# Kernel tuning notes

Measured on AMD Instinct MI355X. Metric: run time of the kernel, lower is better.

The kernel has to match this reference:

```python
import jax, jax.numpy as jnp
import numpy as np

B, S, DIM, DA = 64, 4096, 256, 64
NEG = -1e30

def setup_inputs() -> dict:
    key = jax.random.key(0)
    k1, k2, k3, k4 = jax.random.split(key, 4)
    h = jax.random.normal(k1, (B, S, DIM), dtype=jnp.float32)
    mask = jax.random.randint(k2, (B, S), 0, 2).astype(jnp.bool_)
    # xavier_uniform with gain=1.414 as in the torch module
    lim_a = 1.414 * np.sqrt(6.0 / (DIM + DA))
    lim_b = 1.414 * np.sqrt(6.0 / (DA + 1))
    a = jax.random.uniform(k3, (DIM, DA), minval=-lim_a, maxval=lim_a, dtype=jnp.float32)
    b = jax.random.uniform(k4, (DA, 1), minval=-lim_b, maxval=lim_b, dtype=jnp.float32)
    return {"h": h, "mask": mask, "a": a, "b": b}

def reference(h, mask, a, b):
    # e: (B, S) additive-attention logits
    e = jnp.einsum('bsk,ko->bs', jnp.tanh(jnp.einsum('bsd,dk->bsk', h, a)), b)
    e = e + mask.astype(e.dtype) * NEG  # True == padding -> -1e30
    attn = jax.nn.softmax(e, axis=1)    # softmax over seq dim
    # weighted sum over seq: (B, DIM)
    return jnp.einsum('bs,bsd->bd', attn, h)
```

## Files before the change

kernel.cpp:

```cpp
#include <hip/hip_runtime.h>
#include <hip/hip_bf16.h>

#define B_      64
#define S_      4096
#define DIM_    256
#define DA_     64
#define NEG_    (-1e30f)
#define CHUNKS_ 16
#define ROWS_   256
#define NBLK_   256
#define TILES_TOT_ 16
#define LDW_    260
#define PSTR_   258

typedef _Float16 half8 __attribute__((ext_vector_type(8)));
typedef float float4v __attribute__((ext_vector_type(4)));

__device__ __forceinline__ float tanh_fast(float x) {
    float e = __expf(2.0f * x);
    return 1.0f - 2.0f * __builtin_amdgcn_rcpf(e + 1.0f);
}

__global__ __launch_bounds__(256) void prep_kernel(
    const float* __restrict__ a, const void* __restrict__ mask,
    _Float16* __restrict__ at_sw, int* __restrict__ flag)
{
    int idx = blockIdx.x * 256 + threadIdx.x;
    int j    = idx & 7;
    int lane = (idx >> 3) & 63;
    int kbnt = idx >> 9;
    int kb   = kbnt & 7;
    int nt   = kbnt >> 3;
    int d  = kb * 32 + (lane >> 4) * 8 + j;
    int kf = nt * 16 + (lane & 15);
    at_sw[idx] = (_Float16)a[d * DA_ + kf];

    if (blockIdx.x == 0) {
        __shared__ int anynz;
        if (threadIdx.x == 0) anynz = 0;
        __syncthreads();
        const unsigned char* mb = (const unsigned char*)mask;
        int base = threadIdx.x * 4;
        int v = mb[base + 1] | mb[base + 2] | mb[base + 3];
        if (v) atomicOr(&anynz, 1);
        __syncthreads();
        if (threadIdx.x == 0) *flag = (anynz == 0) ? 1 : 0;
    }
}

#define STAGE(ft_, sel_) do {                                                   \
    int cg_ = (int)blockIdx.x + ((ft_) >> 2) * NBLK_;                           \
    long long r0_ = (long long)(cg_ >> 4) * S_ + (long long)(cg_ & 15) * ROWS_  \
                  + ((ft_) & 3) * 64 + wave * 16;                               \
    const float* sp_ = h + r0_ * DIM_ + lane * 4;                               \
    _Pragma("unroll")                                                           \
    for (int i_ = 0; i_ < 16; ++i_) {                                           \
        __builtin_amdgcn_global_load_lds(                                       \
            (__attribute__((address_space(1))) void*)(sp_ + (size_t)i_ * DIM_), \
            (__attribute__((address_space(3))) void*)&buf[sel_][wave * 16 + i_][0], \
            16, 0, 0);                                                          \
    }                                                                           \
} while (0)

__global__ __launch_bounds__(256, 1) void fused_kernel(
    const float* __restrict__ h, const _Float16* __restrict__ at_sw,
    const float* __restrict__ bvec, const void* __restrict__ mask,
    const int* __restrict__ flag, float* __restrict__ part)
{
    __shared__ float buf[2][64][LDW_];

    const int t    = threadIdx.x;
    const int wave = t >> 6;
    const int lane = t & 63;
    const int quad = lane >> 4;
    const int nrow = lane & 15;
    const bool int32enc = (*flag != 0);

    half8 af[4][8];
    #pragma unroll
    for (int nt = 0; nt < 4; ++nt)
        #pragma unroll
        for (int kb = 0; kb < 8; ++kb)
            af[nt][kb] = *(const half8*)(at_sw + ((nt * 8 + kb) * 64 + lane) * 8);

    float4 bq[4];
    #pragma unroll
    for (int nt = 0; nt < 4; ++nt)
        bq[nt] = *(const float4*)(bvec + nt * 16 + quad * 4);

    float acc0 = 0.f, acc1 = 0.f, acc2 = 0.f, acc3 = 0.f;
    float m_w = NEG_, l_w = 0.f;

    STAGE(0, 0);
    asm volatile("s_waitcnt vmcnt(0)" ::: "memory");
    __builtin_amdgcn_sched_barrier(0);

    int cur = 0;
    #pragma unroll 1
    for (int ft = 0; ft < TILES_TOT_; ++ft) {
        int cg = (int)blockIdx.x + (ft >> 2) * NBLK_;
        long long row0 = (long long)(cg >> 4) * S_ + (long long)(cg & 15) * ROWS_
                       + (ft & 3) * 64 + wave * 16;

        long long mrow = row0 + nrow;
        int mv = int32enc ? ((const int*)mask)[mrow]
                          : (int)((const unsigned char*)mask)[mrow];

        if (ft < TILES_TOT_ - 1) STAGE(ft + 1, cur ^ 1);

        const float* hrow_l = &buf[cur][wave * 16 + nrow][0];
        float4v accm[4];
        #pragma unroll
        for (int nt = 0; nt < 4; ++nt) accm[nt] = (float4v){0.f, 0.f, 0.f, 0.f};
        #pragma unroll
        for (int kb = 0; kb < 8; ++kb) {
            float4 ha = *(const float4*)(hrow_l + kb * 32 + quad * 8);
            float4 hb2 = *(const float4*)(hrow_l + kb * 32 + quad * 8 + 4);
            union { _Float16 hh[8]; half8 v; } pk;
            pk.hh[0] = (_Float16)ha.x;  pk.hh[1] = (_Float16)ha.y;
            pk.hh[2] = (_Float16)ha.z;  pk.hh[3] = (_Float16)ha.w;
            pk.hh[4] = (_Float16)hb2.x; pk.hh[5] = (_Float16)hb2.y;
            pk.hh[6] = (_Float16)hb2.z; pk.hh[7] = (_Float16)hb2.w;
            #pragma unroll
            for (int nt = 0; nt < 4; ++nt)
                accm[nt] = __builtin_amdgcn_mfma_f32_16x16x32_f16(af[nt][kb], pk.v, accm[nt], 0, 0, 0);
        }

        float p = 0.f;
        #pragma unroll
        for (int nt = 0; nt < 4; ++nt) {
            p += tanh_fast(accm[nt][0]) * bq[nt].x;
            p += tanh_fast(accm[nt][1]) * bq[nt].y;
            p += tanh_fast(accm[nt][2]) * bq[nt].z;
            p += tanh_fast(accm[nt][3]) * bq[nt].w;
        }
        p += __shfl_xor(p, 16);
        p += __shfl_xor(p, 32);

        float ev = mv ? NEG_ : p;
        float mx = ev;
        mx = fmaxf(mx, __shfl_xor(mx, 1));
        mx = fmaxf(mx, __shfl_xor(mx, 2));
        mx = fmaxf(mx, __shfl_xor(mx, 4));
        mx = fmaxf(mx, __shfl_xor(mx, 8));
        float m_new = fmaxf(m_w, mx);
        float rs  = __expf(m_w - m_new);
        float w_s = __expf(ev - m_new);
        float sm = w_s;
        sm += __shfl_xor(sm, 1);
        sm += __shfl_xor(sm, 2);
        sm += __shfl_xor(sm, 4);
        sm += __shfl_xor(sm, 8);
        l_w = l_w * rs + sm;
        m_w = m_new;
        acc0 *= rs; acc1 *= rs; acc2 *= rs; acc3 *= rs;

        #pragma unroll
        for (int s = 0; s < 16; ++s) {
            float wv = __shfl(w_s, s);
            float4 hv = *(const float4*)(&buf[cur][wave * 16 + s][lane * 4]);
            acc0 = fmaf(wv, hv.x, acc0);
            acc1 = fmaf(wv, hv.y, acc1);
            acc2 = fmaf(wv, hv.z, acc2);
            acc3 = fmaf(wv, hv.w, acc3);
        }

        if ((ft & 3) == 3) {
            float* pc = part + (size_t)(cg * 4 + wave) * PSTR_;
            float4 o4 = make_float4(acc0, acc1, acc2, acc3);
            *(float4*)(pc + 2 + lane * 4) = o4;
            if (lane == 0) { pc[0] = m_w; pc[1] = l_w; }
            acc0 = acc1 = acc2 = acc3 = 0.f;
            m_w = NEG_; l_w = 0.f;
        }

        asm volatile("s_waitcnt vmcnt(0) lgkmcnt(0)" ::: "memory");
        __builtin_amdgcn_sched_barrier(0);
        cur ^= 1;
    }
}

__global__ __launch_bounds__(256) void merge_kernel(
    const float* __restrict__ part, float* __restrict__ out)
{
    const int b = blockIdx.x;
    const int t = threadIdx.x;
    const float* pb = part + (size_t)b * 64 * PSTR_;
    float M = NEG_;
    #pragma unroll
    for (int i = 0; i < 64; ++i) M = fmaxf(M, pb[i * PSTR_]);
    float L = 0.f, o = 0.f;
    #pragma unroll
    for (int i = 0; i < 64; ++i) {
        float sc = __expf(pb[i * PSTR_] - M);
        L += pb[i * PSTR_ + 1] * sc;
        o += pb[i * PSTR_ + 2 + t] * sc;
    }
    out[b * DIM_ + t] = o / L;
}

extern "C" void kernel_launch(void* const* d_in, const int* in_sizes, int n_in,
                              void* d_out, int out_size, void* d_ws, size_t ws_size,
                              hipStream_t stream) {
    const float* h    = (const float*)d_in[0];
    const void*  mask = d_in[1];
    const float* a    = (const float*)d_in[2];
    const float* bvec = (const float*)d_in[3];
    float* out = (float*)d_out;

    char* ws = (char*)d_ws;
    _Float16* at_sw = (_Float16*)ws;
    int* flag       = (int*)(ws + 32768);
    float* part     = (float*)(ws + 36864);

    prep_kernel<<<64, 256, 0, stream>>>(a, mask, at_sw, flag);
    fused_kernel<<<NBLK_, 256, 0, stream>>>(h, at_sw, bvec, mask, flag, part);
    merge_kernel<<<B_, 256, 0, stream>>>(part, out);
}
```

Before: 370.5 us.

## Launch one block per chunk with single LDS buffer and on-the-fly weight loads

Replaces the persistent 256-block grid (each block looping over 16 tiles with double-buffered LDS) with 1024 blocks, each handling one 256-row chunk in four sequential tiles with a single LDS buffer and no prefetch. The A-matrix fragments are now read from global memory inside the MFMA loop instead of being held in registers, and launch bounds allow two blocks per CU. The intent is to hide memory latency through occupancy rather than explicit double buffering. In exchange it loses the copy/compute overlap inside each block and adds repeated global/L1 loads of the weights. The partial-record stride is padded so the float4 store is aligned.

```diff
diff --git a/kernel.cpp b/kernel.cpp
--- a/kernel.cpp
+++ b/kernel.cpp
@@ -8,10 +8,8 @@
 #define NEG_    (-1e30f)
 #define CHUNKS_ 16
 #define ROWS_   256
-#define NBLK_   256
-#define TILES_TOT_ 16
 #define LDW_    260
-#define PSTR_   258
+#define PSTR_   264
 
 typedef _Float16 half8 __attribute__((ext_vector_type(8)));
 typedef float float4v __attribute__((ext_vector_type(4)));
@@ -48,26 +46,23 @@
     }
 }
 
-#define STAGE(ft_, sel_) do {                                                   \
-    int cg_ = (int)blockIdx.x + ((ft_) >> 2) * NBLK_;                           \
-    long long r0_ = (long long)(cg_ >> 4) * S_ + (long long)(cg_ & 15) * ROWS_  \
-                  + ((ft_) & 3) * 64 + wave * 16;                               \
-    const float* sp_ = h + r0_ * DIM_ + lane * 4;                               \
+#define STAGE(tile_) do {                                                       \
+    const float* sp_ = h + (crow + (tile_) * 64 + wave * 16) * DIM_ + lane * 4; \
     _Pragma("unroll")                                                           \
     for (int i_ = 0; i_ < 16; ++i_) {                                           \
         __builtin_amdgcn_global_load_lds(                                       \
             (__attribute__((address_space(1))) void*)(sp_ + (size_t)i_ * DIM_), \
-            (__attribute__((address_space(3))) void*)&buf[sel_][wave * 16 + i_][0], \
+            (__attribute__((address_space(3))) void*)&buf[wave * 16 + i_][0],   \
             16, 0, 0);                                                          \
     }                                                                           \
 } while (0)
 
-__global__ __launch_bounds__(256, 1) void fused_kernel(
+__global__ __launch_bounds__(256, 2) void fused_kernel(
     const float* __restrict__ h, const _Float16* __restrict__ at_sw,
     const float* __restrict__ bvec, const void* __restrict__ mask,
     const int* __restrict__ flag, float* __restrict__ part)
 {
-    __shared__ float buf[2][64][LDW_];
+    __shared__ float buf[64][LDW_];
 
     const int t    = threadIdx.x;
     const int wave = t >> 6;
@@ -76,45 +71,39 @@
     const int nrow = lane & 15;
     const bool int32enc = (*flag != 0);
 
-    half8 af[4][8];
-    #pragma unroll
-    for (int nt = 0; nt < 4; ++nt)
-        #pragma unroll
-        for (int kb = 0; kb < 8; ++kb)
-            af[nt][kb] = *(const half8*)(at_sw + ((nt * 8 + kb) * 64 + lane) * 8);
-
     float4 bq[4];
     #pragma unroll
     for (int nt = 0; nt < 4; ++nt)
         bq[nt] = *(const float4*)(bvec + nt * 16 + quad * 4);
 
+    const int cg = blockIdx.x;
+    const long long crow = (long long)(cg >> 4) * S_ + (cg & 15) * ROWS_;
+    const long long row0 = crow + wave * 16 + nrow;
+
+    int mv0, mv1, mv2, mv3;
+    if (int32enc) {
+        const int* mi = (const int*)mask + row0;
+        mv0 = mi[0]; mv1 = mi[64]; mv2 = mi[128]; mv3 = mi[192];
+    } else {
+        const unsigned char* mb = (const unsigned char*)mask + row0;
+        mv0 = mb[0]; mv1 = mb[64]; mv2 = mb[128]; mv3 = mb[192];
+    }
+
     float acc0 = 0.f, acc1 = 0.f, acc2 = 0.f, acc3 = 0.f;
     float m_w = NEG_, l_w = 0.f;
 
-    STAGE(0, 0);
-    asm volatile("s_waitcnt vmcnt(0)" ::: "memory");
-    __builtin_amdgcn_sched_barrier(0);
-
-    int cur = 0;
-    #pragma unroll 1
-    for (int ft = 0; ft < TILES_TOT_; ++ft) {
-        int cg = (int)blockIdx.x + (ft >> 2) * NBLK_;
-        long long row0 = (long long)(cg >> 4) * S_ + (long long)(cg & 15) * ROWS_
-                       + (ft & 3) * 64 + wave * 16;
-
-        long long mrow = row0 + nrow;
-        int mv = int32enc ? ((const int*)mask)[mrow]
-                          : (int)((const unsigned char*)mask)[mrow];
-
-        if (ft < TILES_TOT_ - 1) STAGE(ft + 1, cur ^ 1);
-
-        const float* hrow_l = &buf[cur][wave * 16 + nrow][0];
+    auto body = [&](int tile, int mv) {
+        STAGE(tile);
+        asm volatile("s_waitcnt vmcnt(0)" ::: "memory");
+        __builtin_amdgcn_sched_barrier(0);
+
+        const float* hrow_l = &buf[wave * 16 + nrow][0];
         float4v accm[4];
         #pragma unroll
         for (int nt = 0; nt < 4; ++nt) accm[nt] = (float4v){0.f, 0.f, 0.f, 0.f};
         #pragma unroll
         for (int kb = 0; kb < 8; ++kb) {
-            float4 ha = *(const float4*)(hrow_l + kb * 32 + quad * 8);
+            float4 ha  = *(const float4*)(hrow_l + kb * 32 + quad * 8);
             float4 hb2 = *(const float4*)(hrow_l + kb * 32 + quad * 8 + 4);
             union { _Float16 hh[8]; half8 v; } pk;
             pk.hh[0] = (_Float16)ha.x;  pk.hh[1] = (_Float16)ha.y;
@@ -122,8 +111,10 @@
             pk.hh[4] = (_Float16)hb2.x; pk.hh[5] = (_Float16)hb2.y;
             pk.hh[6] = (_Float16)hb2.z; pk.hh[7] = (_Float16)hb2.w;
             #pragma unroll
-            for (int nt = 0; nt < 4; ++nt)
-                accm[nt] = __builtin_amdgcn_mfma_f32_16x16x32_f16(af[nt][kb], pk.v, accm[nt], 0, 0, 0);
+            for (int nt = 0; nt < 4; ++nt) {
+                half8 af = *(const half8*)(at_sw + ((nt * 8 + kb) * 64 + lane) * 8);
+                accm[nt] = __builtin_amdgcn_mfma_f32_16x16x32_f16(af, pk.v, accm[nt], 0, 0, 0);
+            }
         }
 
         float p = 0.f;
@@ -158,26 +149,18 @@
         #pragma unroll
         for (int s = 0; s < 16; ++s) {
             float wv = __shfl(w_s, s);
-            float4 hv = *(const float4*)(&buf[cur][wave * 16 + s][lane * 4]);
+            float4 hv = *(const float4*)(&buf[wave * 16 + s][lane * 4]);
             acc0 = fmaf(wv, hv.x, acc0);
             acc1 = fmaf(wv, hv.y, acc1);
             acc2 = fmaf(wv, hv.z, acc2);
             acc3 = fmaf(wv, hv.w, acc3);
         }
-
-        if ((ft & 3) == 3) {
-            float* pc = part + (size_t)(cg * 4 + wave) * PSTR_;
-            float4 o4 = make_float4(acc0, acc1, acc2, acc3);
-            *(float4*)(pc + 2 + lane * 4) = o4;
-            if (lane == 0) { pc[0] = m_w; pc[1] = l_w; }
-            acc0 = acc1 = acc2 = acc3 = 0.f;
-            m_w = NEG_; l_w = 0.f;
-        }
-
-        asm volatile("s_waitcnt vmcnt(0) lgkmcnt(0)" ::: "memory");
-        __builtin_amdgcn_sched_barrier(0);
-        cur ^= 1;
-    }
+    };
+    body(0, mv0); body(1, mv1); body(2, mv2); body(3, mv3);
+
+    float* pc = part + (size_t)(cg * 4 + wave) * PSTR_;
+    *(float4*)(pc + 4 + lane * 4) = make_float4(acc0, acc1, acc2, acc3);
+    if (lane == 0) { pc[0] = m_w; pc[1] = l_w; }
 }
 
 __global__ __launch_bounds__(256) void merge_kernel(
@@ -194,7 +177,7 @@
     for (int i = 0; i < 64; ++i) {
         float sc = __expf(pb[i * PSTR_] - M);
         L += pb[i * PSTR_ + 1] * sc;
-        o += pb[i * PSTR_ + 2 + t] * sc;
+        o += pb[i * PSTR_ + 4 + t] * sc;
     }
     out[b * DIM_ + t] = o / L;
 }
@@ -214,6 +197,6 @@
     float* part     = (float*)(ws + 36864);
 
     prep_kernel<<<64, 256, 0, stream>>>(a, mask, at_sw, flag);
-    fused_kernel<<<NBLK_, 256, 0, stream>>>(h, at_sw, bvec, mask, flag, part);
+    fused_kernel<<<B_ * CHUNKS_, 256, 0, stream>>>(h, at_sw, bvec, mask, flag, part);
     merge_kernel<<<B_, 256, 0, stream>>>(part, out);
 }
```

New measurement: 371.8 us. About the same (+0.4%).
